# Optimization experiments

Hardware: AMD Instinct MI355X
Metric: run time of the kernel (lower is better)

The kernel has to match this reference:

```python
import jax, jax.numpy as jnp
import numpy as np

NY, NU, NH = 64, 64, 256  # Nhidden=256 -> 128 complex eigen pairs
T, NB = 4096, 32          # horizon, batch


def setup_inputs() -> dict:
    key = jax.random.key(0)
    ks = jax.random.split(key, 9)
    return {
        "y0": jax.random.normal(ks[0], (NB, NY), jnp.float32),
        "U": jax.random.normal(ks[1], (T, NB, NU), jnp.float32),
        "lmbd_cont_real": jax.random.uniform(ks[2], (NH // 2,), jnp.float32),
        "lmbd_cont_imag": jax.random.uniform(ks[3], (NH // 2,), jnp.float32),
        "B": jax.random.normal(ks[4], (NH, NU), jnp.float32) / np.sqrt(NU),
        "W_y2x": jax.random.normal(ks[5], (NH, NY), jnp.float32) / np.sqrt(NY),
        "b_y2x": jax.random.normal(ks[6], (NH,), jnp.float32) * 0.01,
        "W_x2y": jax.random.normal(ks[7], (NY, NH), jnp.float32) / np.sqrt(NH),
        "b_x2y": jax.random.normal(ks[8], (NY,), jnp.float32) * 0.01,
    }


def reference(y0, U, lmbd_cont_real, lmbd_cont_imag, B, W_y2x, b_y2x, W_x2y, b_x2y):
    # where A is the real 2x2-block form of complex eigenvalues
    # lambda = r * exp(i*theta), r = exp(-|re|), theta = (pi/2)*im.
    # Original builds A^n explicitly (O(T^2)); an O(T) scan computes the same math.
    H = B.shape[0] // 2
    Bu = jnp.einsum('tbu,hu->tbh', U, B)          # (T, NB, NH)
    r = jnp.exp(-jnp.abs(lmbd_cont_real))
    theta = (jnp.pi / 2) * lmbd_cont_imag
    lr = r * jnp.cos(theta)                        # Re(lambda), (H,)
    li = r * jnp.sin(theta)                        # Im(lambda), (H,)
    x0 = y0 @ W_y2x.T + b_y2x                      # (NB, NH)
    zr0, zi0 = x0[:, :H], x0[:, H:]
    a, b = Bu[:, :, :H], Bu[:, :, H:]

    def step(carry, inp):
        zr, zi = carry
        ak, bk = inp
        nzr = lr * zr - li * zi + ak
        nzi = li * zr + lr * zi + bk
        return (nzr, nzi), (nzr, nzi)

    _, (Xr, Xi) = jax.lax.scan(step, (zr0, zi0), (a, b))
    X = jnp.concatenate([Xr, Xi], axis=-1)         # (T, NB, NH)
    Y = X @ W_x2y.T + b_x2y                        # (T, NB, NY)
    return Y
```

## Files before the change

### kernel.cpp

```cpp
#include <hip/hip_runtime.h>
#include <math.h>

#define TT   4096
#define NBB  32
#define NUU  64
#define NHH  256
#define HH   128
#define NYY  64
#define LCH  8
#define CCH  512
#define SEGN 16
#define CPS  32

#define PI_HALF 1.5707963267948966f

typedef float  f32x16 __attribute__((ext_vector_type(16)));
typedef __bf16 bf16x8 __attribute__((ext_vector_type(8)));
typedef __bf16 bf16x2 __attribute__((ext_vector_type(2)));
typedef unsigned int uint4v __attribute__((ext_vector_type(4)));

__device__ inline int crow(int r, int lane) { return (r & 3) + 8 * (r >> 2) + 4 * (lane >> 5); }
__device__ inline bf16x8 ldfrag(const unsigned short* p) {
    return __builtin_bit_cast(bf16x8, *(const uint4v*)p);
}

#define CVT(v, H, L) { __bf16 _h = (__bf16)(v); H = _h; L = (__bf16)((v) - (float)_h); }

__device__ inline void lam_f32(float xre, float xim, float& lr, float& li) {
    float th = PI_HALF * xim;
    float rf = (float)exp(-(double)fabsf(xre));
    float cf = (float)cos((double)th);
    float sf = (float)sin((double)th);
    lr = rf * cf; li = rf * sf;
}

__device__ inline int swzU(int row, int so) {
    return row * 128 + ((((so >> 3) ^ row) & 15) << 3) + (so & 7);
}
__device__ inline int swzX(int row, int so) {
    int chv = so >> 3;
    chv = (chv & 32) | ((chv ^ row) & 31);
    return row * 512 + (chv << 3) + (so & 7);
}

__global__ __launch_bounds__(256) void k_prep(
    const float* __restrict__ B, const float* __restrict__ W,
    const float* __restrict__ y0, const float* __restrict__ Wy2x,
    const float* __restrict__ by2x,
    const float* __restrict__ lre, const float* __restrict__ lim,
    unsigned short* __restrict__ Bph, unsigned short* __restrict__ Bpl,
    unsigned short* __restrict__ Wph, unsigned short* __restrict__ Wpl,
    unsigned short* __restrict__ Bq2h, unsigned short* __restrict__ Bq2l,
    float2* __restrict__ x0p)
{
    int bx = blockIdx.x, tid = threadIdx.x;
    if (bx < 32) {
        if (tid < HH) {
            int b = bx, ch = tid;
            float xr = by2x[ch], xi = by2x[ch + HH];
            for (int y = 0; y < NYY; ++y) {
                float v = y0[b * NYY + y];
                xr += v * Wy2x[ch * NYY + y];
                xi += v * Wy2x[(ch + HH) * NYY + y];
            }
            x0p[b * HH + ch] = make_float2(xr, xi);
        }
    } else if (bx < 96) {
        int i = (bx - 32) * 256 + tid;
        float bv = B[i];
        __bf16 bh = (__bf16)bv;
        Bph[i] = __builtin_bit_cast(unsigned short, bh);
        Bpl[i] = __builtin_bit_cast(unsigned short, (__bf16)(bv - (float)bh));
        int y = i >> 8, kidx = i & 255;
        float wv = W[y * NHH + (kidx & 1) * HH + (kidx >> 1)];
        __bf16 wh = (__bf16)wv;
        Wph[i] = __builtin_bit_cast(unsigned short, wh);
        Wpl[i] = __builtin_bit_cast(unsigned short, (__bf16)(wv - (float)wh));
    } else {
        int F = (bx - 96) * 256 + tid;
        int lane = F & 63, kk = (F >> 6) & 31, w = (F >> 11) & 3, nt = (F >> 13) & 1;
        int l31 = lane & 31, kh = lane >> 5;
        int ch = w * 32 + l31;
        int kb = kk * 16 + kh * 8;
        int j = kb >> 6;
        float lrf, lif; lam_f32(lre[ch], lim[ch], lrf, lif);
        double pr = 1.0, pi_ = 0.0;
        for (int s = 0; s < 7 - j; ++s) {
            double nr = pr * (double)lrf - pi_ * (double)lif;
            double ni = pr * (double)lif + pi_ * (double)lrf;
            pr = nr; pi_ = ni;
        }
        for (int e = 0; e < 8; ++e) {
            int u = (kb + e) & 63;
            double b0 = (double)B[ch * NUU + u];
            double b1 = (double)B[(ch + HH) * NUU + u];
            float val = (nt == 0) ? (float)(pr * b0 - pi_ * b1)
                                  : (float)(pi_ * b0 + pr * b1);
            __bf16 vh = (__bf16)val;
            Bq2h[(size_t)F * 8 + e] = __builtin_bit_cast(unsigned short, vh);
            Bq2l[(size_t)F * 8 + e] = __builtin_bit_cast(unsigned short, (__bf16)(val - (float)vh));
        }
    }
}

__global__ __launch_bounds__(256, 1) void k_pass1(
    const float* __restrict__ U,
    const unsigned short* __restrict__ Bq2h, const unsigned short* __restrict__ Bq2l,
    float2* __restrict__ E)
{
    __shared__ __align__(16) unsigned short sL[32 * 1024];

    const int tid = threadIdx.x, w = tid >> 6, lane = tid & 63;
    const int l31 = lane & 31, kh = lane >> 5;
    const int c = blockIdx.x;
    const int ch = w * 32 + l31;

#pragma unroll
    for (int p = 0; p < 4; ++p) {
        int flat0 = p * 4096 + tid * 16;
        const float4* sp = (const float4*)(U + (size_t)c * 16384 + flat0);
        float4 f0 = sp[0], f1 = sp[1], f2 = sp[2], f3 = sp[3];
        int j = flat0 >> 11, b = (flat0 >> 6) & 31, u0 = flat0 & 63;
        bf16x8 h0, h1, l0, l1;
        CVT(f0.x, h0[0], l0[0]); CVT(f0.y, h0[1], l0[1]); CVT(f0.z, h0[2], l0[2]); CVT(f0.w, h0[3], l0[3]);
        CVT(f1.x, h0[4], l0[4]); CVT(f1.y, h0[5], l0[5]); CVT(f1.z, h0[6], l0[6]); CVT(f1.w, h0[7], l0[7]);
        CVT(f2.x, h1[0], l1[0]); CVT(f2.y, h1[1], l1[1]); CVT(f2.z, h1[2], l1[2]); CVT(f2.w, h1[3], l1[3]);
        CVT(f3.x, h1[4], l1[4]); CVT(f3.y, h1[5], l1[5]); CVT(f3.z, h1[6], l1[6]); CVT(f3.w, h1[7], l1[7]);
        int m  = b & 15;
        int cA = ((j * 8 + (u0 >> 3))     ^ m);
        int cB = ((j * 8 + (u0 >> 3) + 1) ^ m);
        *(bf16x8*)&sL[b * 1024 + cA * 8]       = h0;
        *(bf16x8*)&sL[b * 1024 + cB * 8]       = h1;
        *(bf16x8*)&sL[b * 1024 + 512 + cA * 8] = l0;
        *(bf16x8*)&sL[b * 1024 + 512 + cB * 8] = l1;
    }
    __syncthreads();

    const unsigned short* b0h = Bq2h + ((size_t)(0 + w) * 32) * 512 + lane * 8;
    const unsigned short* b1h = Bq2h + ((size_t)(4 + w) * 32) * 512 + lane * 8;
    const unsigned short* b0l = Bq2l + ((size_t)(0 + w) * 32) * 512 + lane * 8;
    const unsigned short* b1l = Bq2l + ((size_t)(4 + w) * 32) * 512 + lane * 8;

    f32x16 acc0, acc1;
#pragma unroll
    for (int r = 0; r < 16; ++r) { acc0[r] = 0.f; acc1[r] = 0.f; }

    const int m = l31 & 15;
    const int rowb = l31 * 1024;
#pragma unroll 4
    for (int kk = 0; kk < 32; ++kk) {
        int chs = ((kk * 2 + kh) ^ m) * 8;
        bf16x8 ah  = ldfrag(&sL[rowb + chs]);
        bf16x8 al  = ldfrag(&sL[rowb + 512 + chs]);
        bf16x8 bh0 = ldfrag(b0h + (size_t)kk * 512);
        bf16x8 bh1 = ldfrag(b1h + (size_t)kk * 512);
        bf16x8 bl0 = ldfrag(b0l + (size_t)kk * 512);
        bf16x8 bl1 = ldfrag(b1l + (size_t)kk * 512);
        acc0 = __builtin_amdgcn_mfma_f32_32x32x16_bf16(ah, bh0, acc0, 0, 0, 0);
        acc1 = __builtin_amdgcn_mfma_f32_32x32x16_bf16(ah, bh1, acc1, 0, 0, 0);
        acc0 = __builtin_amdgcn_mfma_f32_32x32x16_bf16(al, bh0, acc0, 0, 0, 0);
        acc1 = __builtin_amdgcn_mfma_f32_32x32x16_bf16(al, bh1, acc1, 0, 0, 0);
        acc0 = __builtin_amdgcn_mfma_f32_32x32x16_bf16(ah, bl0, acc0, 0, 0, 0);
        acc1 = __builtin_amdgcn_mfma_f32_32x32x16_bf16(ah, bl1, acc1, 0, 0, 0);
    }

#pragma unroll
    for (int r = 0; r < 16; ++r)
        E[(size_t)c * 4096 + crow(r, lane) * HH + ch] = make_float2(acc0[r], acc1[r]);
}

__global__ __launch_bounds__(256) void k_cseg(
    const float* __restrict__ lre, const float* __restrict__ lim,
    const float2* __restrict__ E, float2* __restrict__ Esup)
{
    int g = blockIdx.x * 256 + threadIdx.x;
    int chain = g & 4095, seg = g >> 12, ch = chain & 127;
    float lrf, lif; lam_f32(lre[ch], lim[ch], lrf, lif);
    double pr = (double)lrf, pi = (double)lif;
#pragma unroll
    for (int s = 0; s < 3; ++s) { double nr = pr*pr - pi*pi, ni = 2.0*pr*pi; pr = nr; pi = ni; }
    float2 e[CPS];
#pragma unroll
    for (int j = 0; j < CPS; ++j)
        e[j] = E[((size_t)seg * CPS + j) * 4096 + chain];
    double sr = 0.0, si = 0.0;
#pragma unroll
    for (int j = 0; j < CPS; ++j) {
        double nr = pr * sr - pi * si + (double)e[j].x;
        double ni = pi * sr + pr * si + (double)e[j].y;
        sr = nr; si = ni;
    }
    Esup[(size_t)seg * 4096 + chain] = make_float2((float)sr, (float)si);
}

__global__ __launch_bounds__(256) void k_cexp2(
    const float* __restrict__ lre, const float* __restrict__ lim,
    const float2* __restrict__ x0p, const float2* __restrict__ Esup,
    const float2* __restrict__ E, float2* __restrict__ Carry)
{
    int g = blockIdx.x * 256 + threadIdx.x;
    int chain = g & 4095, seg = g >> 12, ch = chain & 127;
    float lrf, lif; lam_f32(lre[ch], lim[ch], lrf, lif);
    double p8r = (double)lrf, p8i = (double)lif;
#pragma unroll
    for (int s = 0; s < 3; ++s) { double nr = p8r*p8r - p8i*p8i, ni = 2.0*p8r*p8i; p8r = nr; p8i = ni; }
    double pr = p8r, pi = p8i;
#pragma unroll
    for (int s = 0; s < 5; ++s) { double nr = pr*pr - pi*pi, ni = 2.0*pr*pi; pr = nr; pi = ni; }
    float2 es[SEGN - 1];
#pragma unroll
    for (int s = 0; s < SEGN - 1; ++s)
        es[s] = Esup[(size_t)s * 4096 + chain];
    float2 c0 = x0p[chain];
    double cr = (double)c0.x, ci = (double)c0.y;
#pragma unroll
    for (int s = 0; s < SEGN - 1; ++s) {
        if (s < seg) {
            double nr = pr * cr - pi * ci + (double)es[s].x;
            double ni = pi * cr + pr * ci + (double)es[s].y;
            cr = nr; ci = ni;
        }
    }
    float2 e[CPS];
#pragma unroll
    for (int j = 0; j < CPS; ++j)
        e[j] = E[((size_t)seg * CPS + j) * 4096 + chain];
#pragma unroll
    for (int j = 0; j < CPS; ++j) {
        Carry[((size_t)seg * CPS + j) * 4096 + chain] = make_float2((float)cr, (float)ci);
        double nr = p8r * cr - p8i * ci + (double)e[j].x;
        double ni = p8i * cr + p8r * ci + (double)e[j].y;
        cr = nr; ci = ni;
    }
}

__global__ __launch_bounds__(256, 1) void k_pass2(
    const float* __restrict__ U,
    const unsigned short* __restrict__ Bph, const unsigned short* __restrict__ Bpl,
    const unsigned short* __restrict__ Wph, const unsigned short* __restrict__ Wpl,
    const float* __restrict__ lre, const float* __restrict__ lim,
    const float* __restrict__ bx2y,
    const float2* __restrict__ Carry, float* __restrict__ Y)
{
    __shared__ __align__(16) unsigned short sU[64 * 128];
    __shared__ __align__(16) unsigned short sX[64 * 512];

    const int tid = threadIdx.x, w = tid >> 6, lane = tid & 63;
    const int l31 = lane & 31, kh = lane >> 5;
    const int c = blockIdx.x;
    const int ch = w * 32 + l31;
    const int mtile = w & 1, ntile = w >> 1;

    float lr, li; lam_f32(lre[ch], lim[ch], lr, li);
    float ybias = bx2y[ntile * 32 + l31];

    bf16x8 bfh[2][4], bfl[2][4];
#pragma unroll
    for (int nt = 0; nt < 2; ++nt)
#pragma unroll
        for (int kk = 0; kk < 4; ++kk) {
            bfh[nt][kk] = ldfrag(&Bph[(size_t)(nt * HH + ch) * NUU + kk * 16 + kh * 8]);
            bfl[nt][kk] = ldfrag(&Bpl[(size_t)(nt * HH + ch) * NUU + kk * 16 + kh * 8]);
        }

    bf16x8 wfh[16], wfl[16];
#pragma unroll
    for (int kk = 0; kk < 16; ++kk) {
        wfh[kk] = ldfrag(&Wph[(size_t)(ntile * 32 + l31) * NHH + kk * 16 + kh * 8]);
        wfl[kk] = ldfrag(&Wpl[(size_t)(ntile * 32 + l31) * NHH + kk * 16 + kh * 8]);
    }

    float zr[16], zi[16];
#pragma unroll
    for (int r = 0; r < 16; ++r) {
        float2 v = Carry[(size_t)c * 4096 + crow(r, lane) * HH + ch];
        zr[r] = v.x; zi[r] = v.y;
    }

    const int srow = tid >> 2, sus = (tid & 3) * 16;
    const int sb = srow & 31, stoff = srow >> 5;
    const float* ubase = U + (size_t)sb * NUU + sus;

    float4 f0, f1, f2, f3;
    {
        const float4* sp = (const float4*)(ubase + (size_t)(c * LCH + stoff) * (NBB * NUU));
        f0 = sp[0]; f1 = sp[1]; f2 = sp[2]; f3 = sp[3];
    }

    for (int sub = 0; sub < 4; ++sub) {
        {
            bf16x8 h0, h1, l0, l1;
            CVT(f0.x, h0[0], l0[0]); CVT(f0.y, h0[1], l0[1]); CVT(f0.z, h0[2], l0[2]); CVT(f0.w, h0[3], l0[3]);
            CVT(f1.x, h0[4], l0[4]); CVT(f1.y, h0[5], l0[5]); CVT(f1.z, h0[6], l0[6]); CVT(f1.w, h0[7], l0[7]);
            CVT(f2.x, h1[0], l1[0]); CVT(f2.y, h1[1], l1[1]); CVT(f2.z, h1[2], l1[2]); CVT(f2.w, h1[3], l1[3]);
            CVT(f3.x, h1[4], l1[4]); CVT(f3.y, h1[5], l1[5]); CVT(f3.z, h1[6], l1[6]); CVT(f3.w, h1[7], l1[7]);
            *(bf16x8*)&sU[swzU(srow, sus)]          = h0;
            *(bf16x8*)&sU[swzU(srow, sus + 8)]      = h1;
            *(bf16x8*)&sU[swzU(srow, 64 + sus)]     = l0;
            *(bf16x8*)&sU[swzU(srow, 64 + sus + 8)] = l1;
        }

        if (sub > 0) {
            f32x16 ya0, ya1, ya2;
#pragma unroll
            for (int r = 0; r < 16; ++r) { ya0[r] = 0.f; ya1[r] = 0.f; ya2[r] = 0.f; }
#pragma unroll
            for (int kk = 0; kk < 16; ++kk) {
                bf16x8 xah = ldfrag(&sX[swzX(mtile * 32 + l31, kk * 16 + kh * 8)]);
                bf16x8 xal = ldfrag(&sX[swzX(mtile * 32 + l31, 256 + kk * 16 + kh * 8)]);
                ya0 = __builtin_amdgcn_mfma_f32_32x32x16_bf16(xah, wfh[kk], ya0, 0, 0, 0);
                ya1 = __builtin_amdgcn_mfma_f32_32x32x16_bf16(xal, wfh[kk], ya1, 0, 0, 0);
                ya2 = __builtin_amdgcn_mfma_f32_32x32x16_bf16(xah, wfl[kk], ya2, 0, 0, 0);
            }
            int t = c * LCH + (sub - 1) * 2 + mtile;
#pragma unroll
            for (int r = 0; r < 16; ++r)
                Y[((size_t)t * NBB + crow(r, lane)) * NYY + ntile * 32 + l31] =
                    (ya0[r] + ya1[r]) + ya2[r] + ybias;
        }
        __syncthreads();

        if (sub < 3) {
            const float4* sp = (const float4*)(ubase + (size_t)(c * LCH + (sub + 1) * 2 + stoff) * (NBB * NUU));
            f0 = sp[0]; f1 = sp[1]; f2 = sp[2]; f3 = sp[3];
        }

        f32x16 acc[2][2];
#pragma unroll
        for (int mt = 0; mt < 2; ++mt)
#pragma unroll
            for (int nt = 0; nt < 2; ++nt)
#pragma unroll
                for (int r = 0; r < 16; ++r) acc[mt][nt][r] = 0.f;

#pragma unroll
        for (int kk = 0; kk < 4; ++kk) {
            bf16x8 a0h = ldfrag(&sU[swzU(l31,      kk * 16 + kh * 8)]);
            bf16x8 a1h = ldfrag(&sU[swzU(32 + l31, kk * 16 + kh * 8)]);
            bf16x8 a0l = ldfrag(&sU[swzU(l31,      64 + kk * 16 + kh * 8)]);
            bf16x8 a1l = ldfrag(&sU[swzU(32 + l31, 64 + kk * 16 + kh * 8)]);
            acc[0][0] = __builtin_amdgcn_mfma_f32_32x32x16_bf16(a0h, bfh[0][kk], acc[0][0], 0, 0, 0);
            acc[0][1] = __builtin_amdgcn_mfma_f32_32x32x16_bf16(a0h, bfh[1][kk], acc[0][1], 0, 0, 0);
            acc[1][0] = __builtin_amdgcn_mfma_f32_32x32x16_bf16(a1h, bfh[0][kk], acc[1][0], 0, 0, 0);
            acc[1][1] = __builtin_amdgcn_mfma_f32_32x32x16_bf16(a1h, bfh[1][kk], acc[1][1], 0, 0, 0);
            acc[0][0] = __builtin_amdgcn_mfma_f32_32x32x16_bf16(a0l, bfh[0][kk], acc[0][0], 0, 0, 0);
            acc[0][1] = __builtin_amdgcn_mfma_f32_32x32x16_bf16(a0l, bfh[1][kk], acc[0][1], 0, 0, 0);
            acc[1][0] = __builtin_amdgcn_mfma_f32_32x32x16_bf16(a1l, bfh[0][kk], acc[1][0], 0, 0, 0);
            acc[1][1] = __builtin_amdgcn_mfma_f32_32x32x16_bf16(a1l, bfh[1][kk], acc[1][1], 0, 0, 0);
            acc[0][0] = __builtin_amdgcn_mfma_f32_32x32x16_bf16(a0h, bfl[0][kk], acc[0][0], 0, 0, 0);
            acc[0][1] = __builtin_amdgcn_mfma_f32_32x32x16_bf16(a0h, bfl[1][kk], acc[0][1], 0, 0, 0);
            acc[1][0] = __builtin_amdgcn_mfma_f32_32x32x16_bf16(a1h, bfl[0][kk], acc[1][0], 0, 0, 0);
            acc[1][1] = __builtin_amdgcn_mfma_f32_32x32x16_bf16(a1h, bfl[1][kk], acc[1][1], 0, 0, 0);
        }

#pragma unroll
        for (int mt = 0; mt < 2; ++mt)
#pragma unroll
            for (int r = 0; r < 16; ++r) {
                float t0 = fmaf(lr, zr[r], acc[mt][0][r]); t0 = fmaf(-li, zi[r], t0);
                float t1 = fmaf(li, zr[r], acc[mt][1][r]); t1 = fmaf(lr, zi[r], t1);
                zr[r] = t0; zi[r] = t1;
                bf16x2 hv, lv;
                { __bf16 _h = (__bf16)t0; hv[0] = _h; lv[0] = (__bf16)(t0 - (float)_h); }
                { __bf16 _h = (__bf16)t1; hv[1] = _h; lv[1] = (__bf16)(t1 - (float)_h); }
                int row = mt * 32 + crow(r, lane);
                *(bf16x2*)&sX[swzX(row, w * 64 + 2 * l31)]       = hv;
                *(bf16x2*)&sX[swzX(row, 256 + w * 64 + 2 * l31)] = lv;
            }
        __syncthreads();
    }

    {
        f32x16 ya0, ya1, ya2;
#pragma unroll
        for (int r = 0; r < 16; ++r) { ya0[r] = 0.f; ya1[r] = 0.f; ya2[r] = 0.f; }
#pragma unroll
        for (int kk = 0; kk < 16; ++kk) {
            bf16x8 xah = ldfrag(&sX[swzX(mtile * 32 + l31, kk * 16 + kh * 8)]);
            bf16x8 xal = ldfrag(&sX[swzX(mtile * 32 + l31, 256 + kk * 16 + kh * 8)]);
            ya0 = __builtin_amdgcn_mfma_f32_32x32x16_bf16(xah, wfh[kk], ya0, 0, 0, 0);
            ya1 = __builtin_amdgcn_mfma_f32_32x32x16_bf16(xal, wfh[kk], ya1, 0, 0, 0);
            ya2 = __builtin_amdgcn_mfma_f32_32x32x16_bf16(xah, wfl[kk], ya2, 0, 0, 0);
        }
        int t = c * LCH + 3 * 2 + mtile;
#pragma unroll
        for (int r = 0; r < 16; ++r)
            Y[((size_t)t * NBB + crow(r, lane)) * NYY + ntile * 32 + l31] =
                (ya0[r] + ya1[r]) + ya2[r] + ybias;
    }
}

extern "C" void kernel_launch(void* const* d_in, const int* in_sizes, int n_in,
                              void* d_out, int out_size, void* d_ws, size_t ws_size,
                              hipStream_t stream) {
    const float* y0    = (const float*)d_in[0];
    const float* U     = (const float*)d_in[1];
    const float* lre   = (const float*)d_in[2];
    const float* lim   = (const float*)d_in[3];
    const float* B     = (const float*)d_in[4];
    const float* W_y2x = (const float*)d_in[5];
    const float* b_y2x = (const float*)d_in[6];
    const float* W_x2y = (const float*)d_in[7];
    const float* b_x2y = (const float*)d_in[8];
    float* Y = (float*)d_out;

    char* p = (char*)d_ws;
    float2* E        = (float2*)p; p += (size_t)CCH * 4096 * sizeof(float2);
    float2* Carry    = (float2*)p; p += (size_t)CCH * 4096 * sizeof(float2);
    float2* Esup     = (float2*)p; p += (size_t)SEGN * 4096 * sizeof(float2);
    float2* x0p      = (float2*)p; p += (size_t)4096 * sizeof(float2);
    unsigned short* Bph  = (unsigned short*)p; p += 16384 * sizeof(unsigned short);
    unsigned short* Bpl  = (unsigned short*)p; p += 16384 * sizeof(unsigned short);
    unsigned short* Wph  = (unsigned short*)p; p += 16384 * sizeof(unsigned short);
    unsigned short* Wpl  = (unsigned short*)p; p += 16384 * sizeof(unsigned short);
    unsigned short* Bq2h = (unsigned short*)p; p += 131072 * sizeof(unsigned short);
    unsigned short* Bq2l = (unsigned short*)p; p += 131072 * sizeof(unsigned short);

    k_prep <<<dim3(160), dim3(256), 0, stream>>>(B, W_x2y, y0, W_y2x, b_y2x,
                                                 lre, lim,
                                                 Bph, Bpl, Wph, Wpl,
                                                 Bq2h, Bq2l, x0p);
    k_pass1<<<dim3(CCH), dim3(256), 0, stream>>>(U, Bq2h, Bq2l, E);
    k_cseg <<<dim3(256), dim3(256), 0, stream>>>(lre, lim, E, Esup);
    k_cexp2<<<dim3(256), dim3(256), 0, stream>>>(lre, lim, x0p, Esup, E, Carry);
    k_pass2<<<dim3(CCH), dim3(256), 0, stream>>>(U, Bph, Bpl, Wph, Wpl, lre, lim, b_x2y, Carry, Y);
}
```

Before: 171.5 us.

## Restructure inter-chunk carry scan into three-level scan with more parallelism

Replaces the two-kernel carry propagation (16 segments of 32 chunks) with three kernels: group sums over 8 chunks, a sequential scan over 64 groups, and a per-chunk fixup that replays up to 7 chunk steps from the group carry. It also precomputes lambda^8 once in the prep kernel instead of recomputing exp/sincos and repeated squaring in every thread. The aim is to expose far more thread parallelism in the carry stages, which were serial and latency bound. In exchange it adds a kernel launch, the middle stage runs only 16 blocks of 64 serial steps, and the fixup rereads E.

Result: slower. 180.2 us (+5.0%).

```diff
diff --git a/kernel.cpp b/kernel.cpp
--- a/kernel.cpp
+++ b/kernel.cpp
@@ -9,8 +9,7 @@
 #define NYY  64
 #define LCH  8
 #define CCH  512
-#define SEGN 16
-#define CPS  32
+#define NGRP 64
 
 #define PI_HALF 1.5707963267948966f
 
@@ -51,7 +50,7 @@
     unsigned short* __restrict__ Bph, unsigned short* __restrict__ Bpl,
     unsigned short* __restrict__ Wph, unsigned short* __restrict__ Wpl,
     unsigned short* __restrict__ Bq2h, unsigned short* __restrict__ Bq2l,
-    float2* __restrict__ x0p)
+    double2* __restrict__ lam8tab, float2* __restrict__ x0p)
 {
     int bx = blockIdx.x, tid = threadIdx.x;
     if (bx < 32) {
@@ -76,7 +75,7 @@
         __bf16 wh = (__bf16)wv;
         Wph[i] = __builtin_bit_cast(unsigned short, wh);
         Wpl[i] = __builtin_bit_cast(unsigned short, (__bf16)(wv - (float)wh));
-    } else {
+    } else if (bx < 160) {
         int F = (bx - 96) * 256 + tid;
         int lane = F & 63, kk = (F >> 6) & 31, w = (F >> 11) & 3, nt = (F >> 13) & 1;
         int l31 = lane & 31, kh = lane >> 5;
@@ -99,6 +98,14 @@
             __bf16 vh = (__bf16)val;
             Bq2h[(size_t)F * 8 + e] = __builtin_bit_cast(unsigned short, vh);
             Bq2l[(size_t)F * 8 + e] = __builtin_bit_cast(unsigned short, (__bf16)(val - (float)vh));
+        }
+    } else {
+        if (tid < HH) {
+            float lrf, lif; lam_f32(lre[tid], lim[tid], lrf, lif);
+            double pr = (double)lrf, pi_ = (double)lif;
+#pragma unroll
+            for (int s = 0; s < 3; ++s) { double nr = pr*pr - pi_*pi_, ni = 2.0*pr*pi_; pr = nr; pi_ = ni; }
+            lam8tab[tid] = make_double2(pr, pi_);
         }
     }
 }
@@ -169,69 +176,70 @@
         E[(size_t)c * 4096 + crow(r, lane) * HH + ch] = make_float2(acc0[r], acc1[r]);
 }
 
-__global__ __launch_bounds__(256) void k_cseg(
-    const float* __restrict__ lre, const float* __restrict__ lim,
-    const float2* __restrict__ E, float2* __restrict__ Esup)
+__global__ __launch_bounds__(256) void k_cA(
+    const double2* __restrict__ lam8tab,
+    const float2* __restrict__ E, float2* __restrict__ G)
 {
     int g = blockIdx.x * 256 + threadIdx.x;
-    int chain = g & 4095, seg = g >> 12, ch = chain & 127;
-    float lrf, lif; lam_f32(lre[ch], lim[ch], lrf, lif);
-    double pr = (double)lrf, pi = (double)lif;
+    int chain = g & 4095, grp = g >> 12;
+    double2 l8 = lam8tab[chain & 127];
+    float2 e[8];
+#pragma unroll
+    for (int j = 0; j < 8; ++j)
+        e[j] = E[((size_t)grp * 8 + j) * 4096 + chain];
+    double sr = 0.0, si = 0.0;
+#pragma unroll
+    for (int j = 0; j < 8; ++j) {
+        double nr = l8.x * sr - l8.y * si + (double)e[j].x;
+        double ni = l8.y * sr + l8.x * si + (double)e[j].y;
+        sr = nr; si = ni;
+    }
+    G[(size_t)grp * 4096 + chain] = make_float2((float)sr, (float)si);
+}
+
+__global__ __launch_bounds__(256) void k_cB(
+    const double2* __restrict__ lam8tab,
+    const float2* __restrict__ x0p, const float2* __restrict__ G,
+    float2* __restrict__ GC)
+{
+    int chain = blockIdx.x * 256 + threadIdx.x;
+    double2 l8 = lam8tab[chain & 127];
+    double pr = l8.x, pi = l8.y;
 #pragma unroll
     for (int s = 0; s < 3; ++s) { double nr = pr*pr - pi*pi, ni = 2.0*pr*pi; pr = nr; pi = ni; }
-    float2 e[CPS];
-#pragma unroll
-    for (int j = 0; j < CPS; ++j)
-        e[j] = E[((size_t)seg * CPS + j) * 4096 + chain];
-    double sr = 0.0, si = 0.0;
-#pragma unroll
-    for (int j = 0; j < CPS; ++j) {
-        double nr = pr * sr - pi * si + (double)e[j].x;
-        double ni = pi * sr + pr * si + (double)e[j].y;
-        sr = nr; si = ni;
-    }
-    Esup[(size_t)seg * 4096 + chain] = make_float2((float)sr, (float)si);
-}
-
-__global__ __launch_bounds__(256) void k_cexp2(
-    const float* __restrict__ lre, const float* __restrict__ lim,
-    const float2* __restrict__ x0p, const float2* __restrict__ Esup,
-    const float2* __restrict__ E, float2* __restrict__ Carry)
-{
-    int g = blockIdx.x * 256 + threadIdx.x;
-    int chain = g & 4095, seg = g >> 12, ch = chain & 127;
-    float lrf, lif; lam_f32(lre[ch], lim[ch], lrf, lif);
-    double p8r = (double)lrf, p8i = (double)lif;
-#pragma unroll
-    for (int s = 0; s < 3; ++s) { double nr = p8r*p8r - p8i*p8i, ni = 2.0*p8r*p8i; p8r = nr; p8i = ni; }
-    double pr = p8r, pi = p8i;
-#pragma unroll
-    for (int s = 0; s < 5; ++s) { double nr = pr*pr - pi*pi, ni = 2.0*pr*pi; pr = nr; pi = ni; }
-    float2 es[SEGN - 1];
-#pragma unroll
-    for (int s = 0; s < SEGN - 1; ++s)
-        es[s] = Esup[(size_t)s * 4096 + chain];
+    float2 gs[NGRP];
+#pragma unroll
+    for (int g = 0; g < NGRP; ++g)
+        gs[g] = G[(size_t)g * 4096 + chain];
     float2 c0 = x0p[chain];
     double cr = (double)c0.x, ci = (double)c0.y;
 #pragma unroll
-    for (int s = 0; s < SEGN - 1; ++s) {
-        if (s < seg) {
-            double nr = pr * cr - pi * ci + (double)es[s].x;
-            double ni = pi * cr + pr * ci + (double)es[s].y;
-            cr = nr; ci = ni;
-        }
-    }
-    float2 e[CPS];
-#pragma unroll
-    for (int j = 0; j < CPS; ++j)
-        e[j] = E[((size_t)seg * CPS + j) * 4096 + chain];
-#pragma unroll
-    for (int j = 0; j < CPS; ++j) {
-        Carry[((size_t)seg * CPS + j) * 4096 + chain] = make_float2((float)cr, (float)ci);
-        double nr = p8r * cr - p8i * ci + (double)e[j].x;
-        double ni = p8i * cr + p8r * ci + (double)e[j].y;
+    for (int g = 0; g < NGRP; ++g) {
+        GC[(size_t)g * 4096 + chain] = make_float2((float)cr, (float)ci);
+        double nr = pr * cr - pi * ci + (double)gs[g].x;
+        double ni = pi * cr + pr * ci + (double)gs[g].y;
         cr = nr; ci = ni;
     }
+}
+
+__global__ __launch_bounds__(256) void k_cC(
+    const double2* __restrict__ lam8tab,
+    const float2* __restrict__ GC, const float2* __restrict__ E,
+    float2* __restrict__ Carry)
+{
+    int g = blockIdx.x * 256 + threadIdx.x;
+    int chain = g & 4095, c = g >> 12;
+    int grp = c >> 3, o = c & 7;
+    double2 l8 = lam8tab[chain & 127];
+    float2 gc = GC[(size_t)grp * 4096 + chain];
+    double cr = (double)gc.x, ci = (double)gc.y;
+    for (int k = 0; k < o; ++k) {
+        float2 e = E[((size_t)(grp * 8 + k)) * 4096 + chain];
+        double nr = l8.x * cr - l8.y * ci + (double)e.x;
+        double ni = l8.y * cr + l8.x * ci + (double)e.y;
+        cr = nr; ci = ni;
+    }
+    Carry[(size_t)c * 4096 + chain] = make_float2((float)cr, (float)ci);
 }
 
 __global__ __launch_bounds__(256, 1) void k_pass2(
@@ -407,8 +415,10 @@
     char* p = (char*)d_ws;
     float2* E        = (float2*)p; p += (size_t)CCH * 4096 * sizeof(float2);
     float2* Carry    = (float2*)p; p += (size_t)CCH * 4096 * sizeof(float2);
-    float2* Esup     = (float2*)p; p += (size_t)SEGN * 4096 * sizeof(float2);
+    float2* G        = (float2*)p; p += (size_t)NGRP * 4096 * sizeof(float2);
+    float2* GC       = (float2*)p; p += (size_t)NGRP * 4096 * sizeof(float2);
     float2* x0p      = (float2*)p; p += (size_t)4096 * sizeof(float2);
+    double2* lam8tab = (double2*)p; p += (size_t)HH * sizeof(double2);
     unsigned short* Bph  = (unsigned short*)p; p += 16384 * sizeof(unsigned short);
     unsigned short* Bpl  = (unsigned short*)p; p += 16384 * sizeof(unsigned short);
     unsigned short* Wph  = (unsigned short*)p; p += 16384 * sizeof(unsigned short);
@@ -416,12 +426,13 @@
     unsigned short* Bq2h = (unsigned short*)p; p += 131072 * sizeof(unsigned short);
     unsigned short* Bq2l = (unsigned short*)p; p += 131072 * sizeof(unsigned short);
 
-    k_prep <<<dim3(160), dim3(256), 0, stream>>>(B, W_x2y, y0, W_y2x, b_y2x,
+    k_prep <<<dim3(161), dim3(256), 0, stream>>>(B, W_x2y, y0, W_y2x, b_y2x,
                                                  lre, lim,
                                                  Bph, Bpl, Wph, Wpl,
-                                                 Bq2h, Bq2l, x0p);
-    k_pass1<<<dim3(CCH), dim3(256), 0, stream>>>(U, Bq2h, Bq2l, E);
-    k_cseg <<<dim3(256), dim3(256), 0, stream>>>(lre, lim, E, Esup);
-    k_cexp2<<<dim3(256), dim3(256), 0, stream>>>(lre, lim, x0p, Esup, E, Carry);
-    k_pass2<<<dim3(CCH), dim3(256), 0, stream>>>(U, Bph, Bpl, Wph, Wpl, lre, lim, b_x2y, Carry, Y);
-}
+                                                 Bq2h, Bq2l, lam8tab, x0p);
+    k_pass1<<<dim3(CCH),  dim3(256), 0, stream>>>(U, Bq2h, Bq2l, E);
+    k_cA   <<<dim3(1024), dim3(256), 0, stream>>>(lam8tab, E, G);
+    k_cB   <<<dim3(16),   dim3(256), 0, stream>>>(lam8tab, x0p, G, GC);
+    k_cC   <<<dim3(8192), dim3(256), 0, stream>>>(lam8tab, GC, E, Carry);
+    k_pass2<<<dim3(CCH),  dim3(256), 0, stream>>>(U, Bph, Bpl, Wph, Wpl, lre, lim, b_x2y, Carry, Y);
+}
```
